# Kernel optimization log

Hardware: AMD Instinct MI355X
Metric: run time of the kernel (lower is better)

Reference implementation:

```python
import jax, jax.numpy as jnp
from jax import lax
import numpy as np

DEPTH, D_MODEL, D_INNER, D_STATE, DT_RANK = 24, 192, 384, 16, 12
EPS = 1e-5

def _layernorm(x, w, b):
    m = x.mean(-1, keepdims=True)
    v = ((x - m) ** 2).mean(-1, keepdims=True)
    return (x - m) * lax.rsqrt(v + EPS) * w + b

def _silu(x):
    return x * jax.nn.sigmoid(x)

def _mamba_mixer(x, in_w, cw, cb, xp_w, dtw, dtb, a_log, dvec, out_w):
    # x: (B, L, D_MODEL)
    B, L, _ = x.shape
    xz = jnp.einsum('bld,ed->ble', x, in_w)            # (B, L, 2*D_INNER)
    xi, z = xz[..., :D_INNER], xz[..., D_INNER:]
    # causal depthwise conv1d, kernel 4 (left-pad 3, truncate to L)
    xt = jnp.moveaxis(xi, 1, 2)                        # (B, D_INNER, L)
    xt = jnp.pad(xt, ((0, 0), (0, 0), (3, 0)))
    xt = lax.conv_general_dilated(xt, cw[:, None, :], (1,), 'VALID',
                                  dimension_numbers=('NCH', 'OIH', 'NCH'),
                                  feature_group_count=D_INNER)
    xt = _silu(xt + cb[None, :, None])
    xc = jnp.moveaxis(xt, 1, 2)                        # (B, L, D_INNER)
    x_dbl = jnp.einsum('bld,ed->ble', xc, xp_w)        # (B, L, DT_RANK+2*D_STATE)
    dt = x_dbl[..., :DT_RANK]
    Bm = x_dbl[..., DT_RANK:DT_RANK + D_STATE]         # (B, L, N)
    Cm = x_dbl[..., DT_RANK + D_STATE:]                # (B, L, N)
    delta = jax.nn.softplus(jnp.einsum('blr,dr->bld', dt, dtw) + dtb)  # (B, L, D_INNER)
    A = -jnp.exp(a_log)                                # (D_INNER, N)
    dA = jnp.exp(delta[..., None] * A)                 # (B, L, D_INNER, N)
    dBx = (delta * xc)[..., None] * Bm[:, :, None, :]  # (B, L, D_INNER, N)

    def step(h, inp):
        dA_t, dBx_t, C_t = inp
        h = dA_t * h + dBx_t
        y = jnp.einsum('bdn,bn->bd', h, C_t)
        return h, y

    h0 = jnp.zeros((B, D_INNER, D_STATE), x.dtype)
    _, ys = lax.scan(step, h0, (jnp.moveaxis(dA, 1, 0), jnp.moveaxis(dBx, 1, 0), jnp.moveaxis(Cm, 1, 0)))
    y = jnp.moveaxis(ys, 0, 1) + xc * dvec             # (B, L, D_INNER)
    y = y * _silu(z)
    return jnp.einsum('ble,de->bld', y, out_w)

def _forward(x, patch_w, patch_b, norm_w, norm_b, in_proj_w, conv_w, conv_b,
             x_proj_w, dt_w, dt_b, A_log, Dp, out_proj_w, normf_w, normf_b, head_w, head_b):
    # patch embed: conv 16x16 stride 16 -> (B, 192, 14, 14) -> (B, 196, 192)
    h = lax.conv_general_dilated(x, patch_w, (16, 16), 'VALID',
                                 dimension_numbers=('NCHW', 'OIHW', 'NCHW'))
    h = h + patch_b[None, :, None, None]
    B = h.shape[0]
    hidden = h.reshape(B, D_MODEL, -1).transpose(0, 2, 1)  # (B, L, D)
    residual = None
    for d in range(DEPTH):
        residual = hidden if residual is None else residual + hidden
        normed = _layernorm(residual, norm_w[d], norm_b[d])
        hidden = _mamba_mixer(normed, in_proj_w[d], conv_w[d], conv_b[d], x_proj_w[d],
                              dt_w[d], dt_b[d], A_log[d], Dp[d], out_proj_w[d])
    residual = residual + hidden
    feat = _layernorm(residual, normf_w, normf_b)
    pooled = feat.mean(axis=1)                           # final_pool_type='mean'
    return pooled @ head_w.T + head_b                    # (B, num_classes)

def setup_inputs() -> dict:
    key = jax.random.key(0)
    ks = jax.random.split(key, 16)
    s = 0.05
    return {
        'x': jax.random.normal(ks[0], (64, 3, 224, 224), jnp.float32),
        'patch_w': jax.random.normal(ks[1], (192, 3, 16, 16), jnp.float32) * s,
        'patch_b': jnp.zeros((192,), jnp.float32),
        'norm_w': jnp.ones((DEPTH, D_MODEL), jnp.float32),
        'norm_b': jnp.zeros((DEPTH, D_MODEL), jnp.float32),
        'in_proj_w': jax.random.normal(ks[2], (DEPTH, 2 * D_INNER, D_MODEL), jnp.float32) * s,
        'conv_w': jax.random.normal(ks[3], (DEPTH, D_INNER, 4), jnp.float32) * 0.3,
        'conv_b': jnp.zeros((DEPTH, D_INNER), jnp.float32),
        'x_proj_w': jax.random.normal(ks[4], (DEPTH, DT_RANK + 2 * D_STATE, D_INNER), jnp.float32) * s,
        'dt_w': jax.random.normal(ks[5], (DEPTH, D_INNER, DT_RANK), jnp.float32) * s,
        'dt_b': jax.random.uniform(ks[6], (DEPTH, D_INNER), jnp.float32, -4.0, -2.0),
        'A_log': jnp.log(jnp.broadcast_to(jnp.arange(1, D_STATE + 1, dtype=jnp.float32), (DEPTH, D_INNER, D_STATE))),
        'Dp': jnp.ones((DEPTH, D_INNER), jnp.float32),
        'out_proj_w': jax.random.normal(ks[7], (DEPTH, D_MODEL, D_INNER), jnp.float32) * s,
        'normf_w': jnp.ones((D_MODEL,), jnp.float32),
        'normf_b': jnp.zeros((D_MODEL,), jnp.float32),
        'head_w': jax.random.normal(ks[8], (1000, D_MODEL), jnp.float32) * s,
        'head_b': jnp.zeros((1000,), jnp.float32),
    }

def reference(x, patch_w, patch_b, norm_w, norm_b, in_proj_w, conv_w, conv_b,
              x_proj_w, dt_w, dt_b, A_log, Dp, out_proj_w, normf_w, normf_b, head_w, head_b):
    return _forward(x, patch_w, patch_b, norm_w, norm_b, in_proj_w, conv_w, conv_b,
                    x_proj_w, dt_w, dt_b, A_log, Dp, out_proj_w, normf_w, normf_b, head_w, head_b)
```

## Files before the change

kernel.cpp:

```cpp
#include <hip/hip_runtime.h>
#include <math.h>


#define DEPTH 24
#define DM 192
#define DI 384
#define DS 16
#define DR 12
#define SEQL 196
#define BATCH 64
#define MROWS (BATCH*SEQL)
#define XDP 8624
#define LOG2E 1.44269504088896340736f

typedef unsigned short ushort_t;
typedef __bf16 bf16x8 __attribute__((ext_vector_type(8)));
typedef float f32x4 __attribute__((ext_vector_type(4)));

__device__ __forceinline__ float sigmoidf_(float x) { return 1.f / (1.f + __expf(-x)); }

__device__ __forceinline__ ushort_t f2bf(float f) {
    union { float f; unsigned u; } c; c.f = f;
    unsigned u = c.u;
    return (ushort_t)((u + 0x7FFFu + ((u >> 16) & 1u)) >> 16);
}
__device__ __forceinline__ float bf2f(ushort_t u) {
    union { unsigned u; float f; } c; c.u = ((unsigned)u) << 16;
    return c.f;
}

__device__ __forceinline__ void load_lds16(const ushort_t* g, ushort_t* l) {
    __builtin_amdgcn_global_load_lds((__attribute__((address_space(1))) void*)g,
                                     (__attribute__((address_space(3))) void*)l, 16, 0, 0);
}

__global__ void f2bf4_kernel(const float* __restrict__ src, ushort_t* __restrict__ dst, int n4) {
    int i = blockIdx.x * 256 + threadIdx.x;
    if (i >= n4) return;
    float4 v = ((const float4*)src)[i];
    union { ushort_t s[4]; uint2 u; } o;
    o.s[0] = f2bf(v.x); o.s[1] = f2bf(v.y); o.s[2] = f2bf(v.z); o.s[3] = f2bf(v.w);
    ((uint2*)dst)[i] = o.u;
}

__global__ void xp_pad_kernel(const float* __restrict__ src, ushort_t* __restrict__ dst) {
    int i = blockIdx.x * 256 + threadIdx.x;
    if (i >= DEPTH * 64 * 384) return;
    int col = i % 384, row = (i / 384) & 63, d = i / (384 * 64);
    float v = (row < 44) ? src[(size_t)d * 44 * 384 + row * 384 + col] : 0.f;
    dst[i] = f2bf(v);
}

template<bool BF>
__global__ void ln_kernel(float* __restrict__ residual, const float* __restrict__ hidden,
                          const float* __restrict__ w, const float* __restrict__ b,
                          void* __restrict__ out_) {
    int wave = threadIdx.x >> 6, lane = threadIdx.x & 63;
    int row = blockIdx.x * 4 + wave;
    float* rr = residual + (size_t)row * DM;
    const float* hr = hidden + (size_t)row * DM;
    float v0 = rr[lane]       + hr[lane];
    float v1 = rr[lane + 64]  + hr[lane + 64];
    float v2 = rr[lane + 128] + hr[lane + 128];
    rr[lane] = v0; rr[lane + 64] = v1; rr[lane + 128] = v2;
    float s = v0 + v1 + v2;
    #pragma unroll
    for (int off = 32; off > 0; off >>= 1) s += __shfl_down(s, off);
    float mean = __shfl(s, 0) * (1.f / DM);
    float d0 = v0 - mean, d1 = v1 - mean, d2 = v2 - mean;
    float q = d0 * d0 + d1 * d1 + d2 * d2;
    #pragma unroll
    for (int off = 32; off > 0; off >>= 1) q += __shfl_down(q, off);
    float rstd = rsqrtf(__shfl(q, 0) * (1.f / DM) + 1e-5f);
    float o0 = d0 * rstd * w[lane]       + b[lane];
    float o1 = d1 * rstd * w[lane + 64]  + b[lane + 64];
    float o2 = d2 * rstd * w[lane + 128] + b[lane + 128];
    if constexpr (BF) {
        ushort_t* o = (ushort_t*)out_ + (size_t)row * DM;
        o[lane] = f2bf(o0); o[lane + 64] = f2bf(o1); o[lane + 128] = f2bf(o2);
    } else {
        float* o = (float*)out_ + (size_t)row * DM;
        o[lane] = o0; o[lane + 64] = o1; o[lane + 128] = o2;
    }
}

template<int BN, int WM, int WN, int NST, bool TC>
__global__ __launch_bounds__(256, 2) void gemm_mfma(const ushort_t* __restrict__ A,
        const ushort_t* __restrict__ W, float* __restrict__ C, int K, int ldC) {
    constexpr int FM = 128 / (WM * 16);
    constexpr int FN = BN / (WN * 16);
    __shared__ ushort_t sA[128 * 32];
    __shared__ ushort_t sB[BN * 32];
    const int t = threadIdx.x;
    const int wave = t >> 6, lane = t & 63;
    const int lr = lane & 15, lq = lane >> 4;
    const int wr = wave / WN, wc = wave % WN;
    const int m0 = blockIdx.x * 128, n0 = blockIdx.y * BN;
    const int wbase = t & ~63;

    f32x4 acc[FM][FN];
    #pragma unroll
    for (int i = 0; i < FM; i++)
        #pragma unroll
        for (int j = 0; j < FN; j++) acc[i][j] = f32x4{0.f, 0.f, 0.f, 0.f};

    for (int k0 = 0; k0 < K; k0 += 32) {
        __syncthreads();
        #pragma unroll
        for (int c = 0; c < 2; c++) {
            int s = c * 256 + t;
            int row = s >> 2;
            int quad = (s & 3) ^ ((row >> 1) & 3);
            load_lds16(A + (size_t)(m0 + row) * K + k0 + quad * 8,
                       sA + (size_t)(c * 256 + wbase) * 8);
        }
        #pragma unroll
        for (int c = 0; c < BN * 4 / 256; c++) {
            int s = c * 256 + t;
            int row = s >> 2;
            int quad = (s & 3) ^ ((row >> 1) & 3);
            load_lds16(W + (size_t)(n0 + row) * K + k0 + quad * 8,
                       sB + (size_t)(c * 256 + wbase) * 8);
        }
        __syncthreads();
        bf16x8 af[FM], bfr[FN];
        #pragma unroll
        for (int i = 0; i < FM; i++) {
            int row = wr * FM * 16 + i * 16 + lr;
            int slot = (row << 2) | (lq ^ ((row >> 1) & 3));
            af[i] = *(const bf16x8*)&sA[(size_t)slot * 8];
        }
        #pragma unroll
        for (int j = 0; j < FN; j++) {
            int row = wc * FN * 16 + j * 16 + lr;
            int slot = (row << 2) | (lq ^ ((row >> 1) & 3));
            bfr[j] = *(const bf16x8*)&sB[(size_t)slot * 8];
        }
        #pragma unroll
        for (int i = 0; i < FM; i++)
            #pragma unroll
            for (int j = 0; j < FN; j++)
                acc[i][j] = __builtin_amdgcn_mfma_f32_16x16x32_bf16(af[i], bfr[j], acc[i][j], 0, 0, 0);
    }
    int crow0 = m0 + wr * FM * 16 + lq * 4;
    int ccol0 = n0 + wc * FN * 16 + lr;
    if constexpr (TC) {
        #pragma unroll
        for (int i = 0; i < FM; i++) {
            int m = crow0 + i * 16;
            int bb = m / 196, l = m % 196;
            #pragma unroll
            for (int j = 0; j < FN; j++) {
                int col = ccol0 + j * 16;
                if (col < 44) {
                    float4 v = {acc[i][j][0], acc[i][j][1], acc[i][j][2], acc[i][j][3]};
                    *(float4*)(C + (size_t)bb * XDP + (size_t)col * 196 + l) = v;
                }
            }
        }
    } else {
        #pragma unroll
        for (int i = 0; i < FM; i++)
            #pragma unroll
            for (int j = 0; j < FN; j++) {
                if (wc * FN + j >= NST) continue;
                float* cp = C + (size_t)(crow0 + i * 16) * ldC + ccol0 + j * 16;
                #pragma unroll
                for (int r = 0; r < 4; r++) cp[(size_t)r * ldC] = acc[i][j][r];
            }
    }
}

__global__ __launch_bounds__(256, 2) void gemm_patch_mfma(const ushort_t* __restrict__ Xbf,
        const ushort_t* __restrict__ Wbf, const float* __restrict__ bias, float* __restrict__ C) {
    constexpr int FM = 2, FN = 4;
    __shared__ ushort_t sA[128 * 32];
    __shared__ ushort_t sB[64 * 32];
    const int t = threadIdx.x;
    const int wave = t >> 6, lane = t & 63;
    const int lr = lane & 15, lq = lane >> 4;
    const int m0 = blockIdx.x * 128, n0 = blockIdx.y * 64;
    const int wbase = t & ~63;

    const ushort_t* abase[2];
    int aquad[2];
    #pragma unroll
    for (int c = 0; c < 2; c++) {
        int s = c * 256 + t;
        int row = s >> 2;
        aquad[c] = (s & 3) ^ ((row >> 1) & 3);
        int m = m0 + row;
        int b = m / 196, r = m % 196, py = r / 14, px = r % 14;
        abase[c] = Xbf + (size_t)b * 150528 + py * 3584 + px * 16;
    }
    int brow = t >> 2;
    int bquad = (t & 3) ^ ((brow >> 1) & 3);
    const ushort_t* bbase = Wbf + (size_t)(n0 + brow) * 768 + bquad * 8;

    f32x4 acc[FM][FN];
    #pragma unroll
    for (int i = 0; i < FM; i++)
        #pragma unroll
        for (int j = 0; j < FN; j++) acc[i][j] = f32x4{0.f, 0.f, 0.f, 0.f};

    for (int k0 = 0; k0 < 768; k0 += 32) {
        __syncthreads();
        #pragma unroll
        for (int c = 0; c < 2; c++) {
            int k = k0 + aquad[c] * 8;
            int ci = k >> 8, ky = (k >> 4) & 15, kx0 = k & 15;
            load_lds16(abase[c] + ci * 50176 + ky * 224 + kx0,
                       sA + (size_t)(c * 256 + wbase) * 8);
        }
        load_lds16(bbase + k0, sB + (size_t)wbase * 8);
        __syncthreads();
        bf16x8 af[FM], bfr[FN];
        #pragma unroll
        for (int i = 0; i < FM; i++) {
            int row = wave * FM * 16 + i * 16 + lr;
            int slot = (row << 2) | (lq ^ ((row >> 1) & 3));
            af[i] = *(const bf16x8*)&sA[(size_t)slot * 8];
        }
        #pragma unroll
        for (int j = 0; j < FN; j++) {
            int row = j * 16 + lr;
            int slot = (row << 2) | (lq ^ ((row >> 1) & 3));
            bfr[j] = *(const bf16x8*)&sB[(size_t)slot * 8];
        }
        #pragma unroll
        for (int i = 0; i < FM; i++)
            #pragma unroll
            for (int j = 0; j < FN; j++)
                acc[i][j] = __builtin_amdgcn_mfma_f32_16x16x32_bf16(af[i], bfr[j], acc[i][j], 0, 0, 0);
    }
    int crow0 = m0 + wave * FM * 16 + lq * 4;
    int ccol0 = n0 + lr;
    #pragma unroll
    for (int i = 0; i < FM; i++)
        #pragma unroll
        for (int j = 0; j < FN; j++) {
            int col = ccol0 + j * 16;
            float bv = bias[col];
            float* cp = C + (size_t)(crow0 + i * 16) * DM + col;
            #pragma unroll
            for (int r = 0; r < 4; r++) cp[(size_t)r * DM] = acc[i][j][r] + bv;
        }
}

template<bool BIAS>
__global__ __launch_bounds__(256, 2) void gemm64(const float* __restrict__ A,
        const float* __restrict__ W, const float* __restrict__ bias,
        float* __restrict__ C, int M, int N, int K) {
    __shared__ float As[32][68];
    __shared__ float Ws[32][68];
    int t = threadIdx.x;
    int m0 = blockIdx.x * 64, n0 = blockIdx.y * 64;
    int lr = t >> 2, lk = (t & 3) * 4;
    int am = m0 + lr; bool avld = am < M;
    const float* Ap = A + (size_t)(avld ? am : 0) * K + lk;
    int wn = n0 + lr; bool wv = wn < N;
    const float* Wp = W + (size_t)(wv ? wn : 0) * K + lk;
    int tm = (t >> 4) * 4, tn = (t & 15) * 4;
    float acc[4][4];
    #pragma unroll
    for (int i = 0; i < 4; i++)
        #pragma unroll
        for (int j = 0; j < 4; j++) acc[i][j] = 0.f;

    for (int k0 = 0; k0 < K; k0 += 32) {
        float4 a0 = make_float4(0.f, 0.f, 0.f, 0.f), a1 = a0, w0 = a0, w1 = a0;
        if (avld) { a0 = *(const float4*)(Ap + k0); a1 = *(const float4*)(Ap + k0 + 16); }
        if (wv)   { w0 = *(const float4*)(Wp + k0); w1 = *(const float4*)(Wp + k0 + 16); }
        __syncthreads();
        As[lk + 0][lr] = a0.x; As[lk + 1][lr] = a0.y; As[lk + 2][lr] = a0.z; As[lk + 3][lr] = a0.w;
        As[lk + 16][lr] = a1.x; As[lk + 17][lr] = a1.y; As[lk + 18][lr] = a1.z; As[lk + 19][lr] = a1.w;
        Ws[lk + 0][lr] = w0.x; Ws[lk + 1][lr] = w0.y; Ws[lk + 2][lr] = w0.z; Ws[lk + 3][lr] = w0.w;
        Ws[lk + 16][lr] = w1.x; Ws[lk + 17][lr] = w1.y; Ws[lk + 18][lr] = w1.z; Ws[lk + 19][lr] = w1.w;
        __syncthreads();
        #pragma unroll
        for (int kk = 0; kk < 32; kk++) {
            float4 x0 = *(const float4*)&As[kk][tm];
            float4 y0 = *(const float4*)&Ws[kk][tn];
            float av[4] = {x0.x, x0.y, x0.z, x0.w};
            float bv[4] = {y0.x, y0.y, y0.z, y0.w};
            #pragma unroll
            for (int i = 0; i < 4; i++)
                #pragma unroll
                for (int j = 0; j < 4; j++) acc[i][j] = fmaf(av[i], bv[j], acc[i][j]);
        }
    }
    #pragma unroll
    for (int i = 0; i < 4; i++) {
        int m = m0 + tm + i;
        if (m >= M) continue;
        float* cr = C + (size_t)m * N;
        int n = n0 + tn;
        if (n < N) {
            float4 v = {acc[i][0], acc[i][1], acc[i][2], acc[i][3]};
            if (BIAS) { v.x += bias[n]; v.y += bias[n + 1]; v.z += bias[n + 2]; v.w += bias[n + 3]; }
            *(float4*)(cr + n) = v;
        }
    }
}

__global__ void conv_silu_kernel(const float* __restrict__ xz, const float* __restrict__ cw,
                                 const float* __restrict__ cb, ushort_t* __restrict__ xcbf) {
    int idx = blockIdx.x * 256 + threadIdx.x;
    if (idx >= MROWS * DI) return;
    int e = idx % DI; int bl = idx / DI; int l = bl % SEQL; int b = bl / SEQL;
    const float* base = xz + (size_t)(b * SEQL) * 768 + e;
    float w0 = cw[e * 4], w1 = cw[e * 4 + 1], w2 = cw[e * 4 + 2], w3 = cw[e * 4 + 3];
    float acc = cb[e];
    if (l >= 3) acc = fmaf(base[(size_t)(l - 3) * 768], w0, acc);
    if (l >= 2) acc = fmaf(base[(size_t)(l - 2) * 768], w1, acc);
    if (l >= 1) acc = fmaf(base[(size_t)(l - 1) * 768], w2, acc);
    acc = fmaf(base[(size_t)l * 768], w3, acc);
    xcbf[idx] = f2bf(acc * sigmoidf_(acc));
}

__global__ __launch_bounds__(512, 4) void scan_kernel(const float* __restrict__ xdt,
        const ushort_t* __restrict__ xcbf, const float* __restrict__ xz,
        const float* __restrict__ dtw, const float* __restrict__ dtb,
        const float* __restrict__ a_log, const float* __restrict__ Dp, ushort_t* __restrict__ y) {
    __shared__ float sd[44 * 196];
    __shared__ ushort_t zs[8 * 200];
    __shared__ ushort_t xcs[8 * 200];
    __shared__ ushort_t ys[8 * 200];
    __shared__ float avs[8][16];
    __shared__ float wdts[8][16];
    const int b = blockIdx.x, eg = blockIdx.y;
    const int tid = threadIdx.x;
    const int wave = tid >> 6, lane = tid & 63;
    const int e = eg * 8 + wave;

    {
        const float4* src4 = (const float4*)(xdt + (size_t)b * XDP);
        float4* sd4 = (float4*)sd;
        for (int i = tid; i < XDP / 4; i += 512) sd4[i] = src4[i];
    }
    if (lane < DS) avs[wave][lane] = -__expf(a_log[(size_t)e * DS + lane]) * LOG2E;
    if (lane >= 16 && lane < 16 + DR) wdts[wave][lane - 16] = dtw[(size_t)e * DR + (lane - 16)];
    if (tid < 196) {
        int l = tid;
        const ushort_t* xp = xcbf + (size_t)(b * SEQL + l) * DI + eg * 8;
        ushort4 xq0 = *(const ushort4*)xp;
        ushort4 xq1 = *(const ushort4*)(xp + 4);
        const float* zp = xz + (size_t)(b * SEQL + l) * 768 + DI + eg * 8;
        float4 zq0 = *(const float4*)zp;
        float4 zq1 = *(const float4*)(zp + 4);
        xcs[0 * 200 + l] = xq0.x; xcs[1 * 200 + l] = xq0.y;
        xcs[2 * 200 + l] = xq0.z; xcs[3 * 200 + l] = xq0.w;
        xcs[4 * 200 + l] = xq1.x; xcs[5 * 200 + l] = xq1.y;
        xcs[6 * 200 + l] = xq1.z; xcs[7 * 200 + l] = xq1.w;
        zs[0 * 200 + l] = f2bf(zq0.x); zs[1 * 200 + l] = f2bf(zq0.y);
        zs[2 * 200 + l] = f2bf(zq0.z); zs[3 * 200 + l] = f2bf(zq0.w);
        zs[4 * 200 + l] = f2bf(zq1.x); zs[5 * 200 + l] = f2bf(zq1.y);
        zs[6 * 200 + l] = f2bf(zq1.z); zs[7 * 200 + l] = f2bf(zq1.w);
    }
    __syncthreads();

    const float db = dtb[e];
    const bool act = lane < 49;
    const int lbase = act ? lane * 4 : 0;

    f32x4 dt4 = {db, db, db, db};
    #pragma unroll
    for (int k = 0; k < DR; k++) {
        f32x4 r = *(const f32x4*)&sd[k * 196 + lbase];
        dt4 += r * wdts[wave][k];
    }
    f32x4 d4;
    #pragma unroll
    for (int s = 0; s < 4; s++) {
        float v = dt4[s];
        d4[s] = (v > 20.f) ? v : __logf(1.f + __expf(v));
    }
    f32x4 du4;
    {
        ushort4 xcq = *(const ushort4*)&xcs[wave * 200 + lbase];
        du4 = d4 * f32x4{bf2f(xcq.x), bf2f(xcq.y), bf2f(xcq.z), bf2f(xcq.w)};
    }

    float P[DS], h[DS];
    #pragma unroll
    for (int n = 0; n < DS; n++) { P[n] = 1.f; h[n] = 0.f; }
    if (act) {
        #pragma unroll
        for (int n = 0; n < DS; n++) {
            float Avn = avs[wave][n];
            f32x4 Bn = *(const f32x4*)&sd[(12 + n) * 196 + lbase];
            float hn = 0.f, Pn = 1.f;
            #pragma unroll
            for (int s = 0; s < 4; s++) {
                float dA = __builtin_amdgcn_exp2f(d4[s] * Avn);
                hn = fmaf(hn, dA, du4[s] * Bn[s]);
                Pn *= dA;
            }
            P[n] = Pn; h[n] = hn;
        }
    }

    #pragma unroll
    for (int off = 1; off < 64; off <<= 1) {
        #pragma unroll
        for (int n = 0; n < DS; n++) {
            float Pp = __shfl_up(P[n], off);
            float Hp = __shfl_up(h[n], off);
            if (lane >= off) {
                h[n] = fmaf(P[n], Hp, h[n]);
                P[n] *= Pp;
            }
        }
    }
    #pragma unroll
    for (int n = 0; n < DS; n++) {
        float Hp = __shfl_up(h[n], 1);
        h[n] = (lane == 0) ? 0.f : Hp;
    }

    if (act) {
        f32x4 acc4 = {0.f, 0.f, 0.f, 0.f};
        #pragma unroll
        for (int n = 0; n < DS; n++) {
            float Avn = avs[wave][n];
            f32x4 Bn = *(const f32x4*)&sd[(12 + n) * 196 + lbase];
            f32x4 Cn = *(const f32x4*)&sd[(28 + n) * 196 + lbase];
            float hn = h[n];
            #pragma unroll
            for (int s = 0; s < 4; s++) {
                float dA = __builtin_amdgcn_exp2f(d4[s] * Avn);
                hn = fmaf(hn, dA, du4[s] * Bn[s]);
                acc4[s] = fmaf(hn, Cn[s], acc4[s]);
            }
        }
        ushort4 xcq = *(const ushort4*)&xcs[wave * 200 + lbase];
        f32x4 xcv4 = {bf2f(xcq.x), bf2f(xcq.y), bf2f(xcq.z), bf2f(xcq.w)};
        ushort4 zq = *(const ushort4*)&zs[wave * 200 + lbase];
        f32x4 zv4 = {bf2f(zq.x), bf2f(zq.y), bf2f(zq.z), bf2f(zq.w)};
        const float Dv = Dp[e];
        ushort_t* yw = &ys[wave * 200 + lbase];
        #pragma unroll
        for (int s = 0; s < 4; s++) {
            float yv = fmaf(xcv4[s], Dv, acc4[s]);
            float zv = zv4[s];
            yw[s] = f2bf(yv * zv * sigmoidf_(zv));
        }
    }
    __syncthreads();
    if (tid < 196) {
        int l = tid;
        ushort4 o0, o1;
        o0.x = ys[0 * 200 + l]; o0.y = ys[1 * 200 + l];
        o0.z = ys[2 * 200 + l]; o0.w = ys[3 * 200 + l];
        o1.x = ys[4 * 200 + l]; o1.y = ys[5 * 200 + l];
        o1.z = ys[6 * 200 + l]; o1.w = ys[7 * 200 + l];
        ushort_t* yp = y + (size_t)(b * SEQL + l) * DI + eg * 8;
        *(ushort4*)yp = o0;
        *(ushort4*)(yp + 4) = o1;
    }
}

__global__ void pool_kernel(const float* __restrict__ normed, float* __restrict__ pooled) {
    int b = blockIdx.x, d = threadIdx.x;
    float s = 0.f;
    for (int l = 0; l < SEQL; l++) s += normed[(size_t)(b * SEQL + l) * DM + d];
    pooled[b * DM + d] = s * (1.f / 196.f);
}

extern "C" void kernel_launch(void* const* d_in, const int* in_sizes, int n_in,
                              void* d_out, int out_size, void* d_ws, size_t ws_size,
                              hipStream_t stream) {
    const float* x       = (const float*)d_in[0];
    const float* patch_w = (const float*)d_in[1];
    const float* patch_b = (const float*)d_in[2];
    const float* norm_w  = (const float*)d_in[3];
    const float* norm_b  = (const float*)d_in[4];
    const float* in_w    = (const float*)d_in[5];
    const float* conv_w  = (const float*)d_in[6];
    const float* conv_b  = (const float*)d_in[7];
    const float* xp_w    = (const float*)d_in[8];
    const float* dt_w    = (const float*)d_in[9];
    const float* dt_b    = (const float*)d_in[10];
    const float* A_log   = (const float*)d_in[11];
    const float* Dp      = (const float*)d_in[12];
    const float* out_w   = (const float*)d_in[13];
    const float* normf_w = (const float*)d_in[14];
    const float* normf_b = (const float*)d_in[15];
    const float* head_w  = (const float*)d_in[16];
    const float* head_b  = (const float*)d_in[17];

    float* ws = (float*)d_ws;
    float* residual     = ws;
    float* hidden       = ws + 2408448;
    float* xz           = ws + 4816896;
    ushort_t* xcbf      = (ushort_t*)(ws + 14450688);
    ushort_t* y_bf      = (ushort_t*)(ws + 16859136);
    ushort_t* x_bf      = (ushort_t*)(ws + 14450688);
    ushort_t* normed_bf = (ushort_t*)(ws + 19267584);
    float* xdbl_t       = ws + 20471808;
    float* pooled       = ws + 21023744;
    ushort_t* in_w_bf   = (ushort_t*)(ws + 21036032);
    ushort_t* out_w_bf  = (ushort_t*)(ws + 22805504);
    ushort_t* xp_w_bf   = (ushort_t*)(ws + 23690240);
    ushort_t* patch_w_bf= (ushort_t*)(ws + 23985152);

    (void)hipMemsetAsync(residual, 0, (size_t)2408448 * sizeof(float), stream);

    f2bf4_kernel<<<3456, 256, 0, stream>>>(in_w, in_w_bf, 884736);
    f2bf4_kernel<<<1728, 256, 0, stream>>>(out_w, out_w_bf, 442368);
    f2bf4_kernel<<<144, 256, 0, stream>>>(patch_w, patch_w_bf, 36864);
    f2bf4_kernel<<<9408, 256, 0, stream>>>(x, x_bf, 2408448);
    xp_pad_kernel<<<2304, 256, 0, stream>>>(xp_w, xp_w_bf);

    gemm_patch_mfma<<<dim3(98, 3), 256, 0, stream>>>(x_bf, patch_w_bf, patch_b, hidden);

    for (int d = 0; d < DEPTH; ++d) {
        ln_kernel<true><<<3136, 256, 0, stream>>>(residual, hidden, norm_w + d * DM,
                                                  norm_b + d * DM, normed_bf);
        gemm_mfma<192, 2, 2, 12, false><<<dim3(98, 4), 256, 0, stream>>>(normed_bf,
                in_w_bf + (size_t)d * 768 * 192, xz, 192, 768);
        conv_silu_kernel<<<18816, 256, 0, stream>>>(xz, conv_w + d * DI * 4, conv_b + d * DI, xcbf);
        gemm_mfma<64, 4, 1, 3, true><<<dim3(98, 1), 256, 0, stream>>>(xcbf,
                xp_w_bf + (size_t)d * 64 * 384, xdbl_t, 384, 196);
        scan_kernel<<<dim3(64, 48), 512, 0, stream>>>(xdbl_t, xcbf, xz, dt_w + d * DI * DR,
                dt_b + d * DI, A_log + d * DI * DS, Dp + d * DI, y_bf);
        gemm_mfma<64, 4, 1, 4, false><<<dim3(98, 3), 256, 0, stream>>>(y_bf,
                out_w_bf + (size_t)d * 192 * 384, hidden, 384, 192);
    }

    ln_kernel<false><<<3136, 256, 0, stream>>>(residual, hidden, normf_w, normf_b, xz);
    pool_kernel<<<64, 192, 0, stream>>>(xz, pooled);
    gemm64<true><<<dim3(1, 16), 256, 0, stream>>>(pooled, head_w, head_b, (float*)d_out, 64, 1000, 192);
}
```

Baseline: 3.535 ms.

## Store x_proj output as bf16 and recompute scan decay from summed deltas

The x_proj GEMM now writes its transposed dt/B/C output in bf16 instead of fp32. The scan kernel loads it into a bf16 shared-memory buffer, which halves global traffic and LDS footprint for that staging. The cross-lane prefix scan no longer carries a per-state product P of decays. It shuffles one summed delta per lane and recomputes each decay with exp2, cutting shuffles from two per state to one per state plus one. This adds exp2 work in the scan and lowers precision on dt, B and C.

```diff
diff --git a/kernel.cpp b/kernel.cpp
--- a/kernel.cpp
+++ b/kernel.cpp
@@ -27,6 +27,10 @@
 __device__ __forceinline__ float bf2f(ushort_t u) {
     union { unsigned u; float f; } c; c.u = ((unsigned)u) << 16;
     return c.f;
+}
+__device__ __forceinline__ f32x4 bf4tof(const ushort_t* p) {
+    ushort4 q = *(const ushort4*)p;
+    return f32x4{bf2f(q.x), bf2f(q.y), bf2f(q.z), bf2f(q.w)};
 }
 
 __device__ __forceinline__ void load_lds16(const ushort_t* g, ushort_t* l) {
@@ -145,6 +149,7 @@
     int crow0 = m0 + wr * FM * 16 + lq * 4;
     int ccol0 = n0 + wc * FN * 16 + lr;
     if constexpr (TC) {
+        ushort_t* Cb = (ushort_t*)C;
         #pragma unroll
         for (int i = 0; i < FM; i++) {
             int m = crow0 + i * 16;
@@ -153,8 +158,10 @@
             for (int j = 0; j < FN; j++) {
                 int col = ccol0 + j * 16;
                 if (col < 44) {
-                    float4 v = {acc[i][j][0], acc[i][j][1], acc[i][j][2], acc[i][j][3]};
-                    *(float4*)(C + (size_t)bb * XDP + (size_t)col * 196 + l) = v;
+                    ushort4 v;
+                    v.x = f2bf(acc[i][j][0]); v.y = f2bf(acc[i][j][1]);
+                    v.z = f2bf(acc[i][j][2]); v.w = f2bf(acc[i][j][3]);
+                    *(ushort4*)(Cb + (size_t)bb * XDP + (size_t)col * 196 + l) = v;
                 }
             }
         }
@@ -318,11 +325,11 @@
     xcbf[idx] = f2bf(acc * sigmoidf_(acc));
 }
 
-__global__ __launch_bounds__(512, 4) void scan_kernel(const float* __restrict__ xdt,
+__global__ __launch_bounds__(512, 4) void scan_kernel(const ushort_t* __restrict__ xdt,
         const ushort_t* __restrict__ xcbf, const float* __restrict__ xz,
         const float* __restrict__ dtw, const float* __restrict__ dtb,
         const float* __restrict__ a_log, const float* __restrict__ Dp, ushort_t* __restrict__ y) {
-    __shared__ float sd[44 * 196];
+    __shared__ ushort_t sd[44 * 196];
     __shared__ ushort_t zs[8 * 200];
     __shared__ ushort_t xcs[8 * 200];
     __shared__ ushort_t ys[8 * 200];
@@ -334,9 +341,9 @@
     const int e = eg * 8 + wave;
 
     {
-        const float4* src4 = (const float4*)(xdt + (size_t)b * XDP);
-        float4* sd4 = (float4*)sd;
-        for (int i = tid; i < XDP / 4; i += 512) sd4[i] = src4[i];
+        const uint4* src = (const uint4*)(xdt + (size_t)b * XDP);
+        uint4* dst = (uint4*)sd;
+        for (int i = tid; i < XDP / 8; i += 512) dst[i] = src[i];
     }
     if (lane < DS) avs[wave][lane] = -__expf(a_log[(size_t)e * DS + lane]) * LOG2E;
     if (lane >= 16 && lane < 16 + DR) wdts[wave][lane - 16] = dtw[(size_t)e * DR + (lane - 16)];
@@ -366,7 +373,7 @@
     f32x4 dt4 = {db, db, db, db};
     #pragma unroll
     for (int k = 0; k < DR; k++) {
-        f32x4 r = *(const f32x4*)&sd[k * 196 + lbase];
+        f32x4 r = bf4tof(&sd[k * 196 + lbase]);
         dt4 += r * wdts[wave][k];
     }
     f32x4 d4;
@@ -381,36 +388,35 @@
         du4 = d4 * f32x4{bf2f(xcq.x), bf2f(xcq.y), bf2f(xcq.z), bf2f(xcq.w)};
     }
 
-    float P[DS], h[DS];
-    #pragma unroll
-    for (int n = 0; n < DS; n++) { P[n] = 1.f; h[n] = 0.f; }
+    float h[DS];
+    #pragma unroll
+    for (int n = 0; n < DS; n++) h[n] = 0.f;
+    float Dseg = act ? (d4[0] + d4[1] + d4[2] + d4[3]) : 0.f;
     if (act) {
         #pragma unroll
         for (int n = 0; n < DS; n++) {
             float Avn = avs[wave][n];
-            f32x4 Bn = *(const f32x4*)&sd[(12 + n) * 196 + lbase];
-            float hn = 0.f, Pn = 1.f;
+            f32x4 Bn = bf4tof(&sd[(12 + n) * 196 + lbase]);
+            float hn = 0.f;
             #pragma unroll
             for (int s = 0; s < 4; s++) {
                 float dA = __builtin_amdgcn_exp2f(d4[s] * Avn);
                 hn = fmaf(hn, dA, du4[s] * Bn[s]);
-                Pn *= dA;
             }
-            P[n] = Pn; h[n] = hn;
+            h[n] = hn;
         }
     }
 
     #pragma unroll
     for (int off = 1; off < 64; off <<= 1) {
+        float Dprev = __shfl_up(Dseg, off);
         #pragma unroll
         for (int n = 0; n < DS; n++) {
-            float Pp = __shfl_up(P[n], off);
             float Hp = __shfl_up(h[n], off);
-            if (lane >= off) {
-                h[n] = fmaf(P[n], Hp, h[n]);
-                P[n] *= Pp;
-            }
-        }
+            if (lane >= off)
+                h[n] = fmaf(__builtin_amdgcn_exp2f(avs[wave][n] * Dseg), Hp, h[n]);
+        }
+        if (lane >= off) Dseg += Dprev;
     }
     #pragma unroll
     for (int n = 0; n < DS; n++) {
@@ -423,8 +429,8 @@
         #pragma unroll
         for (int n = 0; n < DS; n++) {
             float Avn = avs[wave][n];
-            f32x4 Bn = *(const f32x4*)&sd[(12 + n) * 196 + lbase];
-            f32x4 Cn = *(const f32x4*)&sd[(28 + n) * 196 + lbase];
+            f32x4 Bn = bf4tof(&sd[(12 + n) * 196 + lbase]);
+            f32x4 Cn = bf4tof(&sd[(28 + n) * 196 + lbase]);
             float hn = h[n];
             #pragma unroll
             for (int s = 0; s < 4; s++) {
@@ -497,7 +503,7 @@
     ushort_t* y_bf      = (ushort_t*)(ws + 16859136);
     ushort_t* x_bf      = (ushort_t*)(ws + 14450688);
     ushort_t* normed_bf = (ushort_t*)(ws + 19267584);
-    float* xdbl_t       = ws + 20471808;
+    ushort_t* xdbl_t    = (ushort_t*)(ws + 20471808);
     float* pooled       = ws + 21023744;
     ushort_t* in_w_bf   = (ushort_t*)(ws + 21036032);
     ushort_t* out_w_bf  = (ushort_t*)(ws + 22805504);
@@ -521,7 +527,7 @@
                 in_w_bf + (size_t)d * 768 * 192, xz, 192, 768);
         conv_silu_kernel<<<18816, 256, 0, stream>>>(xz, conv_w + d * DI * 4, conv_b + d * DI, xcbf);
         gemm_mfma<64, 4, 1, 3, true><<<dim3(98, 1), 256, 0, stream>>>(xcbf,
-                xp_w_bf + (size_t)d * 64 * 384, xdbl_t, 384, 196);
+                xp_w_bf + (size_t)d * 64 * 384, (float*)xdbl_t, 384, 196);
         scan_kernel<<<dim3(64, 48), 512, 0, stream>>>(xdbl_t, xcbf, xz, dt_w + d * DI * DR,
                 dt_b + d * DI, A_log + d * DI * DS, Dp + d * DI, y_bf);
         gemm_mfma<64, 4, 1, 4, false><<<dim3(98, 3), 256, 0, stream>>>(y_bf,
```

Measured after the change: 4.256 ms. 20.4% more time.
